# Kernel optimization log

Hardware: AMD Instinct MI355X
Metric: run time of the kernel (lower is better)

The kernel has to match this reference:

```python
import jax, jax.numpy as jnp
import numpy as np

EPS = 1e-4  # matches init_kwargs eps


def setup_inputs() -> dict:
    key = jax.random.key(0)
    k1, k2, k3 = jax.random.split(key, 3)
    B, C, T = 64, 256, 2048
    x = jax.random.normal(k1, (B, C, T), dtype=jnp.float32)
    # per-timestep BatchNorm affine params: [T, C]
    gamma = 1.0 + 0.1 * jax.random.normal(k2, (T, C), dtype=jnp.float32)
    beta = 0.01 * jax.random.normal(k3, (T, C), dtype=jnp.float32)
    return {"x": x, "gamma": gamma, "beta": beta}


def reference(x, gamma, beta):
    # BNTTv1 (training mode): every timestep's BatchNorm1d sees the FULL [B, C, T]
    # tensor, so the batch statistics (per-channel mean/var over B and T) are
    # identical across timesteps. Only the affine (gamma_t, beta_t) differs, and
    # the module keeps just slice t of layer t's output. Equivalent fused form:
    mean = jnp.mean(x, axis=(0, 2), keepdims=True)            # [1, C, 1]
    var = jnp.mean((x - mean) ** 2, axis=(0, 2), keepdims=True)  # biased var
    norm = (x - mean) * jax.lax.rsqrt(var + EPS)              # [B, C, T]
    # gamma/beta: [T, C] -> broadcast as [1, C, T]
    out = norm * gamma.T[None, :, :] + beta.T[None, :, :]
    return out
```

## Files before the change

kernel.cpp:

```cpp
#include <hip/hip_runtime.h>
#include <hip/hip_bf16.h>

#define B_ 64
#define C_ 256
#define T_ 2048
#define EPS_ 1e-4f
#define NPC ((float)(B_ * T_))

#define SPLITS 8
#define BPB (B_ / SPLITS)
#define T4 (T_ / 4)

typedef float f4 __attribute__((ext_vector_type(4)));

__global__ __launch_bounds__(256) void bntt_stats(const float* __restrict__ x,
                                                  float* __restrict__ partials) {
    const int c   = blockIdx.x & (C_ - 1);
    const int s   = blockIdx.x >> 8;
    const int tid = threadIdx.x;

    float sum = 0.0f, sumsq = 0.0f;
    const int b0 = s * BPB;
    #pragma unroll
    for (int b = 0; b < BPB; ++b) {
        const f4* p = (const f4*)(x + (size_t)(b0 + b) * (C_ * T_) + (size_t)c * T_);
        #pragma unroll
        for (int i = 0; i < T4 / 256; ++i) {
            f4 v = p[tid + i * 256];
            sum   += v.x + v.y + v.z + v.w;
            sumsq += v.x * v.x + v.y * v.y + v.z * v.z + v.w * v.w;
        }
    }
    #pragma unroll
    for (int off = 32; off > 0; off >>= 1) {
        sum   += __shfl_down(sum, off);
        sumsq += __shfl_down(sumsq, off);
    }
    __shared__ float ls[4], lss[4];
    const int wave = tid >> 6, lane = tid & 63;
    if (lane == 0) { ls[wave] = sum; lss[wave] = sumsq; }
    __syncthreads();
    if (tid == 0) {
        partials[s * C_ + c]                   = ls[0] + ls[1] + ls[2] + ls[3];
        partials[SPLITS * C_ + s * C_ + c]     = lss[0] + lss[1] + lss[2] + lss[3];
    }
}

__global__ __launch_bounds__(1024) void bntt_prep(const float* __restrict__ gamma,
                                                  const float* __restrict__ beta,
                                                  const float* __restrict__ partials,
                                                  float* __restrict__ scale,
                                                  float* __restrict__ shift) {
    __shared__ float tg[32][33];
    __shared__ float tb[32][33];
    __shared__ float smean[32], sistd[32];
    const int tx = threadIdx.x & 31;
    const int ty = threadIdx.x >> 5;
    const int c0 = blockIdx.x * 32;
    const int t0 = blockIdx.y * 32;

    if (threadIdx.x < 32) {
        const int c = c0 + threadIdx.x;
        float S = 0.0f, SS = 0.0f;
        #pragma unroll
        for (int s = 0; s < SPLITS; ++s) {
            S  += partials[s * C_ + c];
            SS += partials[SPLITS * C_ + s * C_ + c];
        }
        float mean = S / NPC;
        float var  = SS / NPC - mean * mean;
        smean[threadIdx.x] = mean;
        sistd[threadIdx.x] = rsqrtf(var + EPS_);
    }
    tg[ty][tx] = gamma[(size_t)(t0 + ty) * C_ + (c0 + tx)];
    tb[ty][tx] = beta [(size_t)(t0 + ty) * C_ + (c0 + tx)];
    __syncthreads();

    const float mean = smean[ty];
    const float istd = sistd[ty];
    const float sc = tg[tx][ty] * istd;
    scale[(size_t)(c0 + ty) * T_ + (t0 + tx)] = sc;
    shift[(size_t)(c0 + ty) * T_ + (t0 + tx)] = fmaf(-mean, sc, tb[tx][ty]);
}

#define BCHUNK 32
__global__ __launch_bounds__(256) void bntt_norm(const float* __restrict__ x,
                                                 const float* __restrict__ scale,
                                                 const float* __restrict__ shift,
                                                 float* __restrict__ out) {
    const int p   = (blockIdx.x & 511) * 256 + threadIdx.x;
    const int c   = p >> 9;
    const int t4  = p & (T4 - 1);
    const int b0  = (blockIdx.x >> 9) * BCHUNK;

    const f4 sc = ((const f4*)scale)[(size_t)c * T4 + t4];
    const f4 sh = ((const f4*)shift)[(size_t)c * T4 + t4];

    size_t idx = (size_t)(b0 * C_ + c) * T4 + t4;
    const size_t step = (size_t)C_ * T4;
    #pragma unroll 4
    for (int b = 0; b < BCHUNK; ++b) {
        f4 xv = ((const f4*)x)[idx];
        f4 o;
        o.x = fmaf(xv.x, sc.x, sh.x);
        o.y = fmaf(xv.y, sc.y, sh.y);
        o.z = fmaf(xv.z, sc.z, sh.z);
        o.w = fmaf(xv.w, sc.w, sh.w);
        __builtin_nontemporal_store(o, &((f4*)out)[idx]);
        idx += step;
    }
}

__global__ __launch_bounds__(256) void bntt_norm_fb(const float* __restrict__ x,
                                                    const float* __restrict__ gamma,
                                                    const float* __restrict__ beta,
                                                    const float* __restrict__ partials,
                                                    float* __restrict__ out) {
    const int p   = (blockIdx.x & 511) * 256 + threadIdx.x;
    const int c   = p >> 9;
    const int t4  = p & (T4 - 1);
    const int t   = t4 * 4;
    const int b0  = (blockIdx.x >> 9) * BCHUNK;

    float S = 0.0f, SS = 0.0f;
    #pragma unroll
    for (int s = 0; s < SPLITS; ++s) {
        S  += partials[s * C_ + c];
        SS += partials[SPLITS * C_ + s * C_ + c];
    }
    const float mean = S / NPC;
    const float istd = rsqrtf(SS / NPC - mean * mean + EPS_);

    f4 sc, sh;
    #pragma unroll
    for (int j = 0; j < 4; ++j) {
        float g  = gamma[(size_t)(t + j) * C_ + c];
        float bb = beta [(size_t)(t + j) * C_ + c];
        float s1 = g * istd;
        ((float*)&sc)[j] = s1;
        ((float*)&sh)[j] = fmaf(-mean, s1, bb);
    }
    size_t idx = (size_t)(b0 * C_ + c) * T4 + t4;
    const size_t step = (size_t)C_ * T4;
    #pragma unroll 4
    for (int b = 0; b < BCHUNK; ++b) {
        f4 xv = ((const f4*)x)[idx];
        f4 o;
        o.x = fmaf(xv.x, sc.x, sh.x);
        o.y = fmaf(xv.y, sc.y, sh.y);
        o.z = fmaf(xv.z, sc.z, sh.z);
        o.w = fmaf(xv.w, sc.w, sh.w);
        __builtin_nontemporal_store(o, &((f4*)out)[idx]);
        idx += step;
    }
}

extern "C" void kernel_launch(void* const* d_in, const int* in_sizes, int n_in,
                              void* d_out, int out_size, void* d_ws, size_t ws_size,
                              hipStream_t stream) {
    const float* x     = (const float*)d_in[0];
    const float* gamma = (const float*)d_in[1];
    const float* beta  = (const float*)d_in[2];
    float* out = (float*)d_out;

    float* partials = (float*)d_ws;
    float* scale    = partials + 2 * SPLITS * C_;
    float* shift    = scale + (size_t)C_ * T_;
    const size_t need = (2 * SPLITS * C_ + 2 * (size_t)C_ * T_) * sizeof(float);

    bntt_stats<<<C_ * SPLITS, 256, 0, stream>>>(x, partials);

    const int ngrid = (C_ * T4 / 256) * (B_ / BCHUNK);
    if (ws_size >= need) {
        dim3 pg(C_ / 32, T_ / 32);
        bntt_prep<<<pg, 1024, 0, stream>>>(gamma, beta, partials, scale, shift);
        bntt_norm<<<ngrid, 256, 0, stream>>>(x, scale, shift, out);
    } else {
        bntt_norm_fb<<<ngrid, 256, 0, stream>>>(x, gamma, beta, partials, out);
    }
}
```

Before: 252.3 us.

## Fuse stats and normalize into one cooperative kernel with grid sync

Replaces the three-kernel pipeline (stats, scale/shift prep, normalize) with a single cooperative kernel. It computes per-channel partial sums over 4 batch splits, synchronizes the whole grid, then normalizes with gamma/beta read directly in the same blocks. The goal is to remove launch gaps and the scale/shift round trip, and possibly to reuse x from the L2/MALL cache between the phases. The cost is a grid barrier, fewer blocks (1024) that limit parallelism, and strided gamma/beta reads. A two-kernel fallback runs if the cooperative launch fails.

```diff
diff --git a/kernel.cpp b/kernel.cpp
--- a/kernel.cpp
+++ b/kernel.cpp
@@ -1,27 +1,29 @@
 #include <hip/hip_runtime.h>
-#include <hip/hip_bf16.h>
+#include <hip/hip_cooperative_groups.h>
+
+namespace cg = cooperative_groups;
 
 #define B_ 64
 #define C_ 256
 #define T_ 2048
 #define EPS_ 1e-4f
 #define NPC ((float)(B_ * T_))
+#define T4 (T_ / 4)
 
-#define SPLITS 8
+#define SPLITS 4
 #define BPB (B_ / SPLITS)
-#define T4 (T_ / 4)
+#define NBLK 1024
 
 typedef float f4 __attribute__((ext_vector_type(4)));
 
-__global__ __launch_bounds__(256) void bntt_stats(const float* __restrict__ x,
-                                                  float* __restrict__ partials) {
-    const int c   = blockIdx.x & (C_ - 1);
-    const int s   = blockIdx.x >> 8;
-    const int tid = threadIdx.x;
-
+__device__ __forceinline__ void stats_phase(const float* __restrict__ x,
+                                            float* __restrict__ partials,
+                                            int blk, int tid) {
+    const int c = blk & (C_ - 1);
+    const int s = blk >> 8;
     float sum = 0.0f, sumsq = 0.0f;
     const int b0 = s * BPB;
-    #pragma unroll
+    #pragma unroll 4
     for (int b = 0; b < BPB; ++b) {
         const f4* p = (const f4*)(x + (size_t)(b0 + b) * (C_ * T_) + (size_t)c * T_);
         #pragma unroll
@@ -41,86 +43,23 @@
     if (lane == 0) { ls[wave] = sum; lss[wave] = sumsq; }
     __syncthreads();
     if (tid == 0) {
-        partials[s * C_ + c]                   = ls[0] + ls[1] + ls[2] + ls[3];
-        partials[SPLITS * C_ + s * C_ + c]     = lss[0] + lss[1] + lss[2] + lss[3];
+        partials[s * C_ + c]               = ls[0] + ls[1] + ls[2] + ls[3];
+        partials[SPLITS * C_ + s * C_ + c] = lss[0] + lss[1] + lss[2] + lss[3];
+        __threadfence();
     }
 }
 
-__global__ __launch_bounds__(1024) void bntt_prep(const float* __restrict__ gamma,
-                                                  const float* __restrict__ beta,
-                                                  const float* __restrict__ partials,
-                                                  float* __restrict__ scale,
-                                                  float* __restrict__ shift) {
-    __shared__ float tg[32][33];
-    __shared__ float tb[32][33];
-    __shared__ float smean[32], sistd[32];
-    const int tx = threadIdx.x & 31;
-    const int ty = threadIdx.x >> 5;
-    const int c0 = blockIdx.x * 32;
-    const int t0 = blockIdx.y * 32;
-
-    if (threadIdx.x < 32) {
-        const int c = c0 + threadIdx.x;
-        float S = 0.0f, SS = 0.0f;
-        #pragma unroll
-        for (int s = 0; s < SPLITS; ++s) {
-            S  += partials[s * C_ + c];
-            SS += partials[SPLITS * C_ + s * C_ + c];
-        }
-        float mean = S / NPC;
-        float var  = SS / NPC - mean * mean;
-        smean[threadIdx.x] = mean;
-        sistd[threadIdx.x] = rsqrtf(var + EPS_);
-    }
-    tg[ty][tx] = gamma[(size_t)(t0 + ty) * C_ + (c0 + tx)];
-    tb[ty][tx] = beta [(size_t)(t0 + ty) * C_ + (c0 + tx)];
-    __syncthreads();
-
-    const float mean = smean[ty];
-    const float istd = sistd[ty];
-    const float sc = tg[tx][ty] * istd;
-    scale[(size_t)(c0 + ty) * T_ + (t0 + tx)] = sc;
-    shift[(size_t)(c0 + ty) * T_ + (t0 + tx)] = fmaf(-mean, sc, tb[tx][ty]);
-}
-
-#define BCHUNK 32
-__global__ __launch_bounds__(256) void bntt_norm(const float* __restrict__ x,
-                                                 const float* __restrict__ scale,
-                                                 const float* __restrict__ shift,
-                                                 float* __restrict__ out) {
-    const int p   = (blockIdx.x & 511) * 256 + threadIdx.x;
-    const int c   = p >> 9;
-    const int t4  = p & (T4 - 1);
-    const int b0  = (blockIdx.x >> 9) * BCHUNK;
-
-    const f4 sc = ((const f4*)scale)[(size_t)c * T4 + t4];
-    const f4 sh = ((const f4*)shift)[(size_t)c * T4 + t4];
-
-    size_t idx = (size_t)(b0 * C_ + c) * T4 + t4;
-    const size_t step = (size_t)C_ * T4;
-    #pragma unroll 4
-    for (int b = 0; b < BCHUNK; ++b) {
-        f4 xv = ((const f4*)x)[idx];
-        f4 o;
-        o.x = fmaf(xv.x, sc.x, sh.x);
-        o.y = fmaf(xv.y, sc.y, sh.y);
-        o.z = fmaf(xv.z, sc.z, sh.z);
-        o.w = fmaf(xv.w, sc.w, sh.w);
-        __builtin_nontemporal_store(o, &((f4*)out)[idx]);
-        idx += step;
-    }
-}
-
-__global__ __launch_bounds__(256) void bntt_norm_fb(const float* __restrict__ x,
-                                                    const float* __restrict__ gamma,
-                                                    const float* __restrict__ beta,
-                                                    const float* __restrict__ partials,
-                                                    float* __restrict__ out) {
-    const int p   = (blockIdx.x & 511) * 256 + threadIdx.x;
-    const int c   = p >> 9;
-    const int t4  = p & (T4 - 1);
-    const int t   = t4 * 4;
-    const int b0  = (blockIdx.x >> 9) * BCHUNK;
+__device__ __forceinline__ void norm_phase(const float* __restrict__ x,
+                                           const float* __restrict__ gamma,
+                                           const float* __restrict__ beta,
+                                           const float* __restrict__ partials,
+                                           float* __restrict__ out,
+                                           int blk, int tid) {
+    const int half = blk >> 9;
+    const int q    = blk & 511;
+    const int c    = q >> 1;
+    const int t4   = (q & 1) * 256 + tid;
+    const int t    = t4 * 4;
 
     float S = 0.0f, SS = 0.0f;
     #pragma unroll
@@ -140,10 +79,11 @@
         ((float*)&sc)[j] = s1;
         ((float*)&sh)[j] = fmaf(-mean, s1, bb);
     }
-    size_t idx = (size_t)(b0 * C_ + c) * T4 + t4;
+
+    size_t idx = (size_t)((half * (B_ / 2)) * C_ + c) * T4 + t4;
     const size_t step = (size_t)C_ * T4;
     #pragma unroll 4
-    for (int b = 0; b < BCHUNK; ++b) {
+    for (int b = 0; b < B_ / 2; ++b) {
         f4 xv = ((const f4*)x)[idx];
         f4 o;
         o.x = fmaf(xv.x, sc.x, sh.x);
@@ -155,27 +95,44 @@
     }
 }
 
+__global__ __launch_bounds__(256, 4) void bntt_fused(const float* __restrict__ x,
+                                                     const float* __restrict__ gamma,
+                                                     const float* __restrict__ beta,
+                                                     float* __restrict__ partials,
+                                                     float* __restrict__ out) {
+    stats_phase(x, partials, blockIdx.x, threadIdx.x);
+    cg::this_grid().sync();
+    norm_phase(x, gamma, beta, partials, out, blockIdx.x, threadIdx.x);
+}
+
+__global__ __launch_bounds__(256, 4) void bntt_stats_k(const float* __restrict__ x,
+                                                       float* __restrict__ partials) {
+    stats_phase(x, partials, blockIdx.x, threadIdx.x);
+}
+__global__ __launch_bounds__(256, 4) void bntt_norm_k(const float* __restrict__ x,
+                                                      const float* __restrict__ gamma,
+                                                      const float* __restrict__ beta,
+                                                      const float* __restrict__ partials,
+                                                      float* __restrict__ out) {
+    norm_phase(x, gamma, beta, partials, out, blockIdx.x, threadIdx.x);
+}
+
 extern "C" void kernel_launch(void* const* d_in, const int* in_sizes, int n_in,
                               void* d_out, int out_size, void* d_ws, size_t ws_size,
                               hipStream_t stream) {
     const float* x     = (const float*)d_in[0];
     const float* gamma = (const float*)d_in[1];
     const float* beta  = (const float*)d_in[2];
-    float* out = (float*)d_out;
+    float* out      = (float*)d_out;
+    float* partials = (float*)d_ws;
 
-    float* partials = (float*)d_ws;
-    float* scale    = partials + 2 * SPLITS * C_;
-    float* shift    = scale + (size_t)C_ * T_;
-    const size_t need = (2 * SPLITS * C_ + 2 * (size_t)C_ * T_) * sizeof(float);
-
-    bntt_stats<<<C_ * SPLITS, 256, 0, stream>>>(x, partials);
-
-    const int ngrid = (C_ * T4 / 256) * (B_ / BCHUNK);
-    if (ws_size >= need) {
-        dim3 pg(C_ / 32, T_ / 32);
-        bntt_prep<<<pg, 1024, 0, stream>>>(gamma, beta, partials, scale, shift);
-        bntt_norm<<<ngrid, 256, 0, stream>>>(x, scale, shift, out);
-    } else {
-        bntt_norm_fb<<<ngrid, 256, 0, stream>>>(x, gamma, beta, partials, out);
+    void* args[] = {(void*)&x, (void*)&gamma, (void*)&beta,
+                    (void*)&partials, (void*)&out};
+    hipError_t e = hipLaunchCooperativeKernel((const void*)bntt_fused,
+                                              dim3(NBLK), dim3(256),
+                                              args, 0, stream);
+    if (e != hipSuccess) {
+        bntt_stats_k<<<NBLK, 256, 0, stream>>>(x, partials);
+        bntt_norm_k<<<NBLK, 256, 0, stream>>>(x, gamma, beta, partials, out);
     }
 }
```

Measured after the change: 405.3 us. 1.61x slower.
